# Kernel tuning notes

Measured on AMD Instinct MI355X. Metric: run time of the kernel, lower is better.

The kernel has to match this reference:

```python
import jax, jax.numpy as jnp
import numpy as np

S, B, D, H, E, K, FF = 1024, 8, 768, 12, 8, 2, 3072


def _ln(x, w, b, eps=1e-5):
    m = x.mean(-1, keepdims=True)
    v = ((x - m) ** 2).mean(-1, keepdims=True)
    return (x - m) / jnp.sqrt(v + eps) * w + b


def setup_inputs() -> dict:
    key = jax.random.key(0)
    ks = jax.random.split(key, 12)
    s = 0.02
    return {
        "x": jax.random.normal(ks[0], (S, B, D), dtype=jnp.float32),
        "ln1_w": jnp.ones((D,), jnp.float32),
        "ln1_b": jnp.zeros((D,), jnp.float32),
        "in_proj_w": jax.random.normal(ks[1], (3 * D, D), jnp.float32) * s,
        "in_proj_b": jnp.zeros((3 * D,), jnp.float32),
        "out_proj_w": jax.random.normal(ks[2], (D, D), jnp.float32) * s,
        "out_proj_b": jnp.zeros((D,), jnp.float32),
        "ln2_w": jnp.ones((D,), jnp.float32),
        "ln2_b": jnp.zeros((D,), jnp.float32),
        "gate_w": jax.random.normal(ks[3], (E, D), jnp.float32) * s,
        "w1": jax.random.normal(ks[4], (E, D, FF), jnp.float32) * s,
        "b1": jnp.zeros((E, FF), jnp.float32),
        "w2": jax.random.normal(ks[5], (E, FF, D), jnp.float32) * s,
        "b2": jnp.zeros((E, D), jnp.float32),
    }


def reference(x, ln1_w, ln1_b, in_proj_w, in_proj_b, out_proj_w, out_proj_b,
              ln2_w, ln2_b, gate_w, w1, b1, w2, b2):
    s, b, d = x.shape
    hd = d // H
    # --- self attention (nn.MultiheadAttention, seq-first, no mask) ---
    h = _ln(x, ln1_w, ln1_b)
    qkv = h @ in_proj_w.T + in_proj_b            # [S, B, 3D]
    q, k, v = jnp.split(qkv, 3, axis=-1)

    def heads(t):
        return t.reshape(s, b, H, hd).transpose(1, 2, 0, 3)  # [B, H, S, hd]

    q, k, v = heads(q) * (hd ** -0.5), heads(k), heads(v)
    att = jax.nn.softmax(jnp.einsum('bhqd,bhkd->bhqk', q, k), axis=-1)
    o = jnp.einsum('bhqk,bhkd->bhqd', att, v).transpose(2, 0, 1, 3).reshape(s, b, d)
    o = o @ out_proj_w.T + out_proj_b
    x = x + o
    # --- MoE FFN ---
    h2 = _ln(x, ln2_w, ln2_b)
    tok = h2.reshape(-1, d)                      # [T, D], T = S*B
    logits = tok @ gate_w.T                      # [T, E]
    rw = jax.nn.softmax(logits.astype(jnp.float32), axis=-1)
    rw_top, sel = jax.lax.top_k(rw, K)           # [T, K]
    rw_top = rw_top / rw_top.sum(-1, keepdims=True)
    rw_top = rw_top.astype(tok.dtype)
    out = jnp.zeros_like(tok)
    for e in range(E):  # small fixed expert loop; math matches gather/scatter dispatch
        we = jnp.where(sel == e, rw_top, 0.0).sum(-1)       # [T] combine weight
        mid = tok @ w1[e] + b1[e]
        mid = mid * jax.nn.sigmoid(1.702 * mid)              # QuickGELU
        out = out + we[:, None] * (mid @ w2[e] + b2[e])
    return x + out.reshape(s, b, d), logits
```

## Files before the change

kernel.cpp:

```cpp
#include <hip/hip_runtime.h>
#include <stdint.h>

#define S_LEN  1024
#define BATCH  8
#define DMODEL 768
#define NHEAD  12
#define HDIM   64
#define NEXP   8
#define FFDIM  3072
#define NTOK   8192
#define D3     2304
#define NGATH  16384
#define MAXWL  136

typedef unsigned short u16;
typedef unsigned int   u32;
typedef __attribute__((ext_vector_type(8))) short bf16x8;
typedef __attribute__((ext_vector_type(4))) float f32x4;
typedef __attribute__((ext_vector_type(4))) short s16x4;

__device__ __forceinline__ u16 f2bf(float f){
  u32 x = __float_as_uint(f);
  x += 0x7fffu + ((x >> 16) & 1u);
  return (u16)(x >> 16);
}
__device__ __forceinline__ float bf2f(u16 u){
  return __uint_as_float(((u32)u) << 16);
}
__device__ __forceinline__ u32 pkbf(float a, float b){
  u32 d; asm("v_cvt_pk_bf16_f32 %0, %1, %2" : "=v"(d) : "v"(a), "v"(b)); return d;
}
__device__ __forceinline__ void gl_lds16(const void* g, void* l){
  __builtin_amdgcn_global_load_lds(
      (const __attribute__((address_space(1))) u32*)(uintptr_t)g,
      (__attribute__((address_space(3))) u32*)(u32)(uintptr_t)l,
      16, 0, 0);
}
__device__ __forceinline__ int swz64(int r){ return ((r & 7) ^ ((r >> 3) & 7)) << 4; }

__device__ __forceinline__ int xcd_swz(int orig, int nwg){
  const int q = nwg >> 3, r = nwg & 7;
  const int xcd = orig & 7, loc = orig >> 3;
  return (xcd < r ? xcd * (q + 1) : r * (q + 1) + (xcd - r) * q) + loc;
}

__global__ __launch_bounds__(256)
void cvt_bf16(const float* __restrict__ in, u16* __restrict__ out, int n)
{
  int i = (blockIdx.x * 256 + threadIdx.x) * 4;
  if (i + 3 < n) {
    float4 v = *(const float4*)(in + i);
    out[i]     = f2bf(v.x);
    out[i + 1] = f2bf(v.y);
    out[i + 2] = f2bf(v.z);
    out[i + 3] = f2bf(v.w);
  }
}

__global__ __launch_bounds__(256)
void transpose_cvt(const float* __restrict__ in, u16* __restrict__ out, int rows, int cols)
{
  __shared__ float tile[64][65];
  const size_t eo = (size_t)blockIdx.z * rows * cols;
  in  += eo; out += eo;
  const int bx = blockIdx.x * 64;
  const int by = blockIdx.y * 64;
  const int tid = threadIdx.x;
  #pragma unroll
  for (int i = 0; i < 4; i++) {
    const int c = tid + 256 * i;
    const int r = c >> 4, c4 = (c & 15) * 4;
    const float4 v = *(const float4*)(in + (size_t)(by + r) * cols + bx + c4);
    tile[r][c4] = v.x; tile[r][c4 + 1] = v.y; tile[r][c4 + 2] = v.z; tile[r][c4 + 3] = v.w;
  }
  __syncthreads();
  #pragma unroll
  for (int i = 0; i < 4; i++) {
    const int c = tid + 256 * i;
    const int orow = c >> 4, r4 = (c & 15) * 4;
    uint2 p;
    p.x = pkbf(tile[r4][orow],     tile[r4 + 1][orow]);
    p.y = pkbf(tile[r4 + 2][orow], tile[r4 + 3][orow]);
    *(uint2*)(out + (size_t)(bx + orow) * rows + by + r4) = p;
  }
}

__global__ __launch_bounds__(256)
void ln_fwd(const float* __restrict__ x, const float* __restrict__ w, const float* __restrict__ b,
            u16* __restrict__ out)
{
  const int t = blockIdx.x, tid = threadIdx.x;
  const float* xr = x + (size_t)t * DMODEL;
  const float v0 = xr[tid], v1 = xr[tid + 256], v2 = xr[tid + 512];
  float s = v0 + v1 + v2, ss = v0 * v0 + v1 * v1 + v2 * v2;
  #pragma unroll
  for (int d = 1; d < 64; d <<= 1) { s += __shfl_xor(s, d); ss += __shfl_xor(ss, d); }
  __shared__ float rs[4], rq[4];
  if ((tid & 63) == 0) { rs[tid >> 6] = s; rq[tid >> 6] = ss; }
  __syncthreads();
  s  = rs[0] + rs[1] + rs[2] + rs[3];
  ss = rq[0] + rq[1] + rq[2] + rq[3];
  const float mean = s * (1.f / DMODEL);
  const float rstd = rsqrtf(ss * (1.f / DMODEL) - mean * mean + 1e-5f);
  u16* orow = out + (size_t)t * DMODEL;
  orow[tid]       = f2bf((v0 - mean) * rstd * w[tid]       + b[tid]);
  orow[tid + 256] = f2bf((v1 - mean) * rstd * w[tid + 256] + b[tid + 256]);
  orow[tid + 512] = f2bf((v2 - mean) * rstd * w[tid + 512] + b[tid + 512]);
}

__global__ __launch_bounds__(256)
void ln2_gate(const float* __restrict__ x1, const float* __restrict__ w, const float* __restrict__ b,
              const float* __restrict__ gate_w, u16* __restrict__ h2,
              float* __restrict__ logits, float* __restrict__ selw, int* __restrict__ seli)
{
  const int t = blockIdx.x, tid = threadIdx.x;
  const float* xr = x1 + (size_t)t * DMODEL;
  const float v0 = xr[tid], v1 = xr[tid + 256], v2 = xr[tid + 512];
  float s = v0 + v1 + v2, ss = v0 * v0 + v1 * v1 + v2 * v2;
  #pragma unroll
  for (int d = 1; d < 64; d <<= 1) { s += __shfl_xor(s, d); ss += __shfl_xor(ss, d); }
  __shared__ float rs[4], rq[4];
  if ((tid & 63) == 0) { rs[tid >> 6] = s; rq[tid >> 6] = ss; }
  __syncthreads();
  s  = rs[0] + rs[1] + rs[2] + rs[3];
  ss = rq[0] + rq[1] + rq[2] + rq[3];
  const float mean = s * (1.f / DMODEL);
  const float rstd = rsqrtf(ss * (1.f / DMODEL) - mean * mean + 1e-5f);
  __shared__ float row[DMODEL];
  const float y0 = (v0 - mean) * rstd * w[tid]       + b[tid];
  const float y1 = (v1 - mean) * rstd * w[tid + 256] + b[tid + 256];
  const float y2 = (v2 - mean) * rstd * w[tid + 512] + b[tid + 512];
  row[tid] = y0; row[tid + 256] = y1; row[tid + 512] = y2;
  u16* hr = h2 + (size_t)t * DMODEL;
  hr[tid] = f2bf(y0); hr[tid + 256] = f2bf(y1); hr[tid + 512] = f2bf(y2);
  __syncthreads();
  __shared__ float lg[NEXP];
  if (tid < 64) {
    const int e = tid >> 3, j = tid & 7;
    const float* gw = gate_w + e * DMODEL;
    float a = 0.f;
    for (int d = j; d < DMODEL; d += 8) a += row[d] * gw[d];
    a += __shfl_xor(a, 1); a += __shfl_xor(a, 2); a += __shfl_xor(a, 4);
    if (j == 0) lg[e] = a;
  }
  __syncthreads();
  if (tid < NEXP) logits[(size_t)t * NEXP + tid] = lg[tid];
  if (tid == 0) {
    int ia = 0, ib = -1;
    float va = -1e30f, vb = -1e30f;
    #pragma unroll
    for (int e = 0; e < NEXP; e++) {
      const float p = lg[e];
      if (p > va)      { vb = va; ib = ia; va = p; ia = e; }
      else if (p > vb) { vb = p; ib = e; }
    }
    const float pb = __expf(vb - va);
    const float inv = 1.f / (1.f + pb);
    selw[2 * t]     = inv;
    selw[2 * t + 1] = pb * inv;
    seli[2 * t]     = ia;
    seli[2 * t + 1] = ib;
  }
}

__global__ __launch_bounds__(256)
void route_count(const int* __restrict__ seli, int* __restrict__ blkcnt)
{
  __shared__ int c[NEXP];
  const int tid = threadIdx.x;
  if (tid < NEXP) c[tid] = 0;
  __syncthreads();
  const int t = blockIdx.x * 256 + tid;
  atomicAdd(&c[seli[2 * t]], 1);
  atomicAdd(&c[seli[2 * t + 1]], 1);
  __syncthreads();
  if (tid < NEXP) blkcnt[blockIdx.x * NEXP + tid] = c[tid];
}

__global__ void route_scan(const int* __restrict__ blkcnt, int* __restrict__ offs,
                           int* __restrict__ blkbase, int* __restrict__ wl, int* __restrict__ nwork)
{
  const int tid = threadIdx.x;
  __shared__ int tot[NEXP];
  __shared__ int off_s[NEXP + 1];
  if (tid < NEXP) {
    int s = 0;
    for (int blk = 0; blk < 32; blk++) s += blkcnt[blk * NEXP + tid];
    tot[tid] = s;
  }
  __syncthreads();
  if (tid == 0) {
    int run = 0;
    for (int e = 0; e < NEXP; e++) { off_s[e] = run; run += tot[e]; }
    off_s[NEXP] = run;
    int nw = 0;
    for (int e = 0; e < NEXP; e++) {
      const int nb = (tot[e] + 127) >> 7;
      for (int i2 = 0; i2 < nb; i2++) wl[nw++] = (e << 16) | i2;
    }
    nwork[0] = nw;
  }
  __syncthreads();
  if (tid <= NEXP) offs[tid] = off_s[tid];
  if (tid < NEXP) {
    int run = off_s[tid];
    for (int blk = 0; blk < 32; blk++) { blkbase[blk * NEXP + tid] = run; run += blkcnt[blk * NEXP + tid]; }
  }
}

__global__ __launch_bounds__(256)
void route_place(const int* __restrict__ seli, const int* __restrict__ blkbase,
                 int* __restrict__ perm, int* __restrict__ posmap)
{
  __shared__ int cnts[2][4][NEXP];
  __shared__ int base[NEXP];
  const int tid = threadIdx.x, l = tid & 63, w = tid >> 6, blk = blockIdx.x;
  const int t = blk * 256 + tid;
  const unsigned long long ltm = (1ull << l) - 1ull;
  int my_e[2], my_r[2];
  my_e[0] = seli[2 * t]; my_e[1] = seli[2 * t + 1];
  my_r[0] = 0; my_r[1] = 0;
  if (tid < NEXP) base[tid] = blkbase[blk * NEXP + tid];
  #pragma unroll
  for (int k = 0; k < 2; k++) {
    #pragma unroll
    for (int ee = 0; ee < NEXP; ee++) {
      const unsigned long long msk = __ballot(my_e[k] == ee);
      if (my_e[k] == ee) my_r[k] = (int)__popcll(msk & ltm);
      if (l == ee) cnts[k][w][ee] = (int)__popcll(msk);
    }
  }
  __syncthreads();
  #pragma unroll
  for (int k = 0; k < 2; k++) {
    const int e = my_e[k];
    int pre = base[e];
    for (int k2 = 0; k2 < 2; k2++)
      for (int w2 = 0; w2 < 4; w2++)
        if (k2 < k || (k2 == k && w2 < w)) pre += cnts[k2][w2][e];
    const int pos = pre + my_r[k];
    perm[pos] = t;
    posmap[2 * t + k] = pos;
  }
}

template<int MODE, int GRP>
__global__ __launch_bounds__(256)
void gemm128(const u16* __restrict__ A, const u16* __restrict__ Bw,
             int M, int N, int Kd,
             const float* __restrict__ bias, const float* __restrict__ resid,
             void* __restrict__ outp,
             const int* __restrict__ perm, const int* __restrict__ offs,
             const int* __restrict__ wl, const int* __restrict__ nwork)
{
  __shared__ u16 As[2][128 * 64];
  __shared__ u16 Bs[2][128 * 64];
  const int tid = threadIdx.x;
  const int l   = tid & 63;
  const int w   = tid >> 6;
  const int wm  = w >> 1, wn = w & 1;

  int gbase = 0, cnt = M, e = 0, bm, bn;
  if (MODE >= 2) {
    const int nw  = nwork[0];
    const int nwg = nw * (N >> 7);
    if ((int)blockIdx.x >= nwg) return;
    const int t    = xcd_swz(blockIdx.x, nwg);
    const int bnin = t % GRP;
    const int q    = t / GRP;
    const int bmi  = q % nw;
    bn = (q / nw) * GRP + bnin;
    const int wk = wl[bmi];
    e  = wk >> 16;
    bm = wk & 0xffff;
    gbase = offs[e];
    cnt   = offs[e + 1] - gbase;
  } else {
    const int nwm = M >> 7;
    const int t    = xcd_swz(blockIdx.x, gridDim.x);
    const int bnin = t % GRP;
    const int q    = t / GRP;
    bm = q % nwm;
    bn = (q / nwm) * GRP + bnin;
  }
  const u16*   Bp = Bw   + (MODE >= 2 ? (size_t)e * N * Kd : 0);
  const float* bp = bias + (MODE >= 2 ? e * N : 0);

  int arow[4], acol[4], brow[4];
  #pragma unroll
  for (int i = 0; i < 4; i++) {
    const int c = tid + 256 * i;
    const int r = c >> 3;
    const int f = (r & 7) ^ ((r >> 3) & 7);
    acol[i] = ((c & 7) ^ f) * 8;
    brow[i] = bn * 128 + r;
    int g;
    if (MODE == 2)      { int gp = gbase + bm * 128 + r; if (gp > NGATH - 1) gp = NGATH - 1; g = perm[gp]; }
    else if (MODE == 3) { int gp = gbase + bm * 128 + r; if (gp > NGATH - 1) gp = NGATH - 1; g = gp; }
    else                g = bm * 128 + r;
    arow[i] = g;
  }

  f32x4 acc[4][4] = {};
  const int nk = Kd >> 6;

  #pragma unroll
  for (int i = 0; i < 4; i++) {
    gl_lds16(A  + (size_t)arow[i] * Kd + acol[i], &As[0][(i * 256 + w * 64) * 8]);
    gl_lds16(Bp + (size_t)brow[i] * Kd + acol[i], &Bs[0][(i * 256 + w * 64) * 8]);
  }

  int cur = 0;
  for (int kt = 0; kt < nk; kt++) {
    const bool pf = (kt + 1 < nk);
    if (pf) {
      const int kb = (kt + 1) * 64;
      #pragma unroll
      for (int i = 0; i < 4; i++) {
        gl_lds16(A  + (size_t)arow[i] * Kd + kb + acol[i], &As[cur ^ 1][(i * 256 + w * 64) * 8]);
        gl_lds16(Bp + (size_t)brow[i] * Kd + kb + acol[i], &Bs[cur ^ 1][(i * 256 + w * 64) * 8]);
      }
      asm volatile("s_waitcnt vmcnt(8)" ::: "memory");
    } else {
      asm volatile("s_waitcnt vmcnt(0)" ::: "memory");
    }
    __builtin_amdgcn_s_barrier();
    __builtin_amdgcn_sched_barrier(0);

    #pragma unroll
    for (int ks = 0; ks < 2; ks++) {
      bf16x8 af[4], bv[4];
      #pragma unroll
      for (int m = 0; m < 4; m++) {
        const int row = wm * 64 + m * 16 + (l & 15);
        af[m] = *(const bf16x8*)((const char*)&As[cur][0] +
                  ((row * 128 + ks * 64 + (l >> 4) * 16) ^ swz64(row)));
      }
      #pragma unroll
      for (int n = 0; n < 4; n++) {
        const int row = wn * 64 + n * 16 + (l & 15);
        bv[n] = *(const bf16x8*)((const char*)&Bs[cur][0] +
                  ((row * 128 + ks * 64 + (l >> 4) * 16) ^ swz64(row)));
      }
      #pragma unroll
      for (int m = 0; m < 4; m++)
        #pragma unroll
        for (int n = 0; n < 4; n++)
          acc[m][n] = __builtin_amdgcn_mfma_f32_16x16x32_bf16(bv[n], af[m], acc[m][n], 0, 0, 0);
    }
    if (pf) __builtin_amdgcn_s_barrier();
    cur ^= 1;
  }

  f32x4 biasv[4];
  int   c0[4];
  #pragma unroll
  for (int n = 0; n < 4; n++) {
    c0[n] = bn * 128 + wn * 64 + n * 16 + ((l >> 4) << 2);
    biasv[n] = *(const f32x4*)(bp + c0[n]);
  }
  #pragma unroll
  for (int m = 0; m < 4; m++) {
    const int row = bm * 128 + wm * 64 + m * 16 + (l & 15);
    #pragma unroll
    for (int n = 0; n < 4; n++) {
      f32x4 v = acc[m][n] + biasv[n];
      if (MODE == 0) {
        *(uint2*)((u16*)outp + (size_t)row * N + c0[n]) =
            make_uint2(pkbf(v[0], v[1]), pkbf(v[2], v[3]));
      } else if (MODE == 1) {
        const size_t o = (size_t)row * N + c0[n];
        f32x4 rv = *(const f32x4*)(resid + o);
        v += rv;
        *(f32x4*)((float*)outp + o) = v;
      } else if (MODE == 2) {
        if (row < cnt) {
          #pragma unroll
          for (int r = 0; r < 4; r++)
            v[r] = v[r] * __builtin_amdgcn_rcpf(1.f + __expf(-1.702f * v[r]));
          *(uint2*)((u16*)outp + (size_t)(gbase + row) * FFDIM + c0[n]) =
              make_uint2(pkbf(v[0], v[1]), pkbf(v[2], v[3]));
        }
      } else {
        if (row < cnt)
          *(uint2*)((u16*)outp + (size_t)(gbase + row) * DMODEL + c0[n]) =
              make_uint2(pkbf(v[0], v[1]), pkbf(v[2], v[3]));
      }
    }
  }
}

__global__ __launch_bounds__(256)
void attn_fwd(const u16* __restrict__ qkv, u16* __restrict__ o)
{
  __shared__ u16 Ksw[64 * 64];
  __shared__ u16 Vt [64 * 64];
  __shared__ u16 Pl [4 * 16 * 64];
  const int tid = threadIdx.x;
  const int l   = tid & 63, w = tid >> 6;
  const int tt  = xcd_swz(blockIdx.x, 16 * BATCH * NHEAD);
  const int qt  = tt & 15;
  const int bh  = tt >> 4;
  const int b_  = bh / NHEAD;
  const int hh  = bh % NHEAD;

  const int qrow = qt * 64 + w * 16 + (l & 15);
  const size_t qoff = ((size_t)(qrow * BATCH + b_)) * D3 + hh * HDIM + (l >> 4) * 8;
  const bf16x8 qa0 = *(const bf16x8*)&qkv[qoff];
  const bf16x8 qa1 = *(const bf16x8*)&qkv[qoff + 32];

  f32x4 oacc[4] = {};
  float m_[4], l_[4];
  #pragma unroll
  for (int r = 0; r < 4; r++) { m_[r] = -1e30f; l_[r] = 0.f; }

  u16* Pw = Pl + w * 1024;
  const int pswz = swz64(l & 15);

  for (int kt = 0; kt < 16; kt++) {
    #pragma unroll
    for (int i = 0; i < 2; i++) {
      const int c = tid + 256 * i;
      const int key = c >> 3, dimb = (c & 7) * 8;
      const size_t gb = ((size_t)((kt * 64 + key) * BATCH + b_)) * D3 + hh * HDIM + dimb;
      const bf16x8 kd = *(const bf16x8*)&qkv[gb + DMODEL];
      const bf16x8 vd = *(const bf16x8*)&qkv[gb + 2 * DMODEL];
      *(bf16x8*)((char*)Ksw + ((key * 128 + dimb * 2) ^ swz64(key))) = kd;
      #pragma unroll
      for (int j = 0; j < 8; j++) {
        const int dim = dimb + j;
        *(u16*)((char*)Vt + ((dim * 128 + key * 2) ^ swz64(dim))) = (u16)vd[j];
      }
    }
    __syncthreads();

    f32x4 sc[4] = {};
    #pragma unroll
    for (int kb2 = 0; kb2 < 4; kb2++) {
      const int key = kb2 * 16 + (l & 15);
      const int ksz = swz64(key);
      #pragma unroll
      for (int ks = 0; ks < 2; ks++) {
        const bf16x8 kf = *(const bf16x8*)((char*)Ksw +
            ((key * 128 + (ks * 32 + (l >> 4) * 8) * 2) ^ ksz));
        sc[kb2] = __builtin_amdgcn_mfma_f32_16x16x32_bf16(ks ? qa1 : qa0, kf, sc[kb2], 0, 0, 0);
      }
    }
    #pragma unroll
    for (int kb2 = 0; kb2 < 4; kb2++)
      #pragma unroll
      for (int r = 0; r < 4; r++) sc[kb2][r] *= 0.125f;

    float nm[4], corr[4], ps[4];
    #pragma unroll
    for (int r = 0; r < 4; r++) {
      float pm = fmaxf(fmaxf(sc[0][r], sc[1][r]), fmaxf(sc[2][r], sc[3][r]));
      pm = fmaxf(pm, __shfl_xor(pm, 1));
      pm = fmaxf(pm, __shfl_xor(pm, 2));
      pm = fmaxf(pm, __shfl_xor(pm, 4));
      pm = fmaxf(pm, __shfl_xor(pm, 8));
      nm[r]   = fmaxf(m_[r], pm);
      corr[r] = __expf(m_[r] - nm[r]);
      m_[r]   = nm[r];
      ps[r]   = 0.f;
    }
    #pragma unroll
    for (int kb2 = 0; kb2 < 4; kb2++) {
      #pragma unroll
      for (int r = 0; r < 4; r++) {
        const float p = __expf(sc[kb2][r] - nm[r]);
        ps[r] += p;
        const int prow = (l >> 4) * 4 + r;
        const int pcol = kb2 * 16 + (l & 15);
        *(u16*)((char*)Pw + ((prow * 128 + pcol * 2) ^ swz64(prow))) = f2bf(p);
      }
    }
    #pragma unroll
    for (int r = 0; r < 4; r++) {
      float s = ps[r];
      s += __shfl_xor(s, 1); s += __shfl_xor(s, 2);
      s += __shfl_xor(s, 4); s += __shfl_xor(s, 8);
      l_[r] = l_[r] * corr[r] + s;
      #pragma unroll
      for (int ob = 0; ob < 4; ob++) oacc[ob][r] *= corr[r];
    }

    #pragma unroll
    for (int ob = 0; ob < 4; ob++) {
      const int dim = ob * 16 + (l & 15);
      const int vsz = swz64(dim);
      #pragma unroll
      for (int ks = 0; ks < 2; ks++) {
        const int kko = (ks * 32 + (l >> 4) * 8) * 2;
        const bf16x8 pf = *(const bf16x8*)((char*)Pw + (((l & 15) * 128 + kko) ^ pswz));
        const bf16x8 vf = *(const bf16x8*)((char*)Vt + ((dim * 128 + kko) ^ vsz));
        oacc[ob] = __builtin_amdgcn_mfma_f32_16x16x32_bf16(pf, vf, oacc[ob], 0, 0, 0);
      }
    }
    __syncthreads();
  }

  #pragma unroll
  for (int r = 0; r < 4; r++) {
    const float inv = 1.f / l_[r];
    const int qs = qt * 64 + w * 16 + (l >> 4) * 4 + r;
    #pragma unroll
    for (int ob = 0; ob < 4; ob++)
      o[((size_t)(qs * BATCH + b_)) * DMODEL + hh * HDIM + ob * 16 + (l & 15)] =
          f2bf(oacc[ob][r] * inv);
  }
}

__global__ __launch_bounds__(192)
void moe_combine(const float* __restrict__ x1, const u16* __restrict__ eout,
                 const int* __restrict__ posmap, const float* __restrict__ selw,
                 float* __restrict__ out)
{
  const int t = blockIdx.x, j = threadIdx.x;
  const int p0 = posmap[2 * t], p1 = posmap[2 * t + 1];
  const float w0 = selw[2 * t], w1 = selw[2 * t + 1];
  const float4 xv = ((const float4*)(x1 + (size_t)t * DMODEL))[j];
  const s16x4 a = ((const s16x4*)(eout + (size_t)p0 * DMODEL))[j];
  const s16x4 c = ((const s16x4*)(eout + (size_t)p1 * DMODEL))[j];
  float4 r;
  r.x = xv.x + w0 * bf2f((u16)a[0]) + w1 * bf2f((u16)c[0]);
  r.y = xv.y + w0 * bf2f((u16)a[1]) + w1 * bf2f((u16)c[1]);
  r.z = xv.z + w0 * bf2f((u16)a[2]) + w1 * bf2f((u16)c[2]);
  r.w = xv.w + w0 * bf2f((u16)a[3]) + w1 * bf2f((u16)c[3]);
  ((float4*)(out + (size_t)t * DMODEL))[j] = r;
}

#define MB (1ull << 20)
static const size_t OFF_H    = 0;
static const size_t OFF_QKV  = 16 * MB;
static const size_t OFF_O    = 54 * MB;
static const size_t OFF_IPW  = 67 * MB;
static const size_t OFF_OPW  = 71 * MB;
static const size_t OFF_MID  = 0;
static const size_t OFF_X1   = 101 * MB;
static const size_t OFF_H2   = 127 * MB;
static const size_t OFF_W1T  = 140 * MB;
static const size_t OFF_W2T  = 178 * MB;
static const size_t OFF_EOUT = 216 * MB;
static const size_t OFF_SELW = 242 * MB;
static const size_t OFF_PERM = 242 * MB + (1 << 16);
static const size_t OFF_POS  = 242 * MB + (2 << 16);
static const size_t OFF_SELI = 242 * MB + (3 << 16);
static const size_t OFF_BCNT = 242 * MB + (4 << 16);
static const size_t OFF_BBASE= 242 * MB + (4 << 16) + 4096;
static const size_t OFF_OFFS = 242 * MB + (4 << 16) + 8192;
static const size_t OFF_WL   = 242 * MB + (5 << 16);
static const size_t OFF_NW   = 242 * MB + (5 << 16) + 1024;

extern "C" void kernel_launch(void* const* d_in, const int* in_sizes, int n_in,
                              void* d_out, int out_size, void* d_ws, size_t ws_size,
                              hipStream_t stream)
{
  const float* x     = (const float*)d_in[0];
  const float* ln1w  = (const float*)d_in[1];
  const float* ln1b  = (const float*)d_in[2];
  const float* ipw_f = (const float*)d_in[3];
  const float* ipb   = (const float*)d_in[4];
  const float* opw_f = (const float*)d_in[5];
  const float* opb   = (const float*)d_in[6];
  const float* ln2w  = (const float*)d_in[7];
  const float* ln2b  = (const float*)d_in[8];
  const float* gatew = (const float*)d_in[9];
  const float* w1    = (const float*)d_in[10];
  const float* b1    = (const float*)d_in[11];
  const float* w2    = (const float*)d_in[12];
  const float* b2    = (const float*)d_in[13];

  char* ws = (char*)d_ws;
  u16*   h    = (u16*)(ws + OFF_H);
  u16*   qkv  = (u16*)(ws + OFF_QKV);
  u16*   ob   = (u16*)(ws + OFF_O);
  u16*   ipw  = (u16*)(ws + OFF_IPW);
  u16*   opw  = (u16*)(ws + OFF_OPW);
  u16*   mid  = (u16*)(ws + OFF_MID);
  float* x1   = (float*)(ws + OFF_X1);
  u16*   h2   = (u16*)(ws + OFF_H2);
  u16*   w1t  = (u16*)(ws + OFF_W1T);
  u16*   w2t  = (u16*)(ws + OFF_W2T);
  u16*   eout = (u16*)(ws + OFF_EOUT);
  float* selw = (float*)(ws + OFF_SELW);
  int*   perm = (int*)(ws + OFF_PERM);
  int*   posm = (int*)(ws + OFF_POS);
  int*   seli = (int*)(ws + OFF_SELI);
  int*   bcnt = (int*)(ws + OFF_BCNT);
  int*   bbas = (int*)(ws + OFF_BBASE);
  int*   offs = (int*)(ws + OFF_OFFS);
  int*   wl   = (int*)(ws + OFF_WL);
  int*   nwork= (int*)(ws + OFF_NW);
  float* outx  = (float*)d_out;
  float* outlg = outx + (size_t)NTOK * DMODEL;

  cvt_bf16<<<(D3 * DMODEL) / 1024, 256, 0, stream>>>(ipw_f, ipw, D3 * DMODEL);
  cvt_bf16<<<(DMODEL * DMODEL) / 1024, 256, 0, stream>>>(opw_f, opw, DMODEL * DMODEL);
  transpose_cvt<<<dim3(FFDIM / 64, DMODEL / 64, NEXP), 256, 0, stream>>>(w1, w1t, DMODEL, FFDIM);
  transpose_cvt<<<dim3(DMODEL / 64, FFDIM / 64, NEXP), 256, 0, stream>>>(w2, w2t, FFDIM, DMODEL);

  ln_fwd<<<NTOK, 256, 0, stream>>>(x, ln1w, ln1b, h);
  gemm128<0, 6><<<(NTOK / 128) * (D3 / 128), 256, 0, stream>>>(
      h, ipw, NTOK, D3, DMODEL, ipb, nullptr, qkv, nullptr, nullptr, nullptr, nullptr);
  attn_fwd<<<(S_LEN / 64) * BATCH * NHEAD, 256, 0, stream>>>(qkv, ob);
  gemm128<1, 6><<<(NTOK / 128) * (DMODEL / 128), 256, 0, stream>>>(
      ob, opw, NTOK, DMODEL, DMODEL, opb, x, x1, nullptr, nullptr, nullptr, nullptr);

  ln2_gate<<<NTOK, 256, 0, stream>>>(x1, ln2w, ln2b, gatew, h2, outlg, selw, seli);
  route_count<<<32, 256, 0, stream>>>(seli, bcnt);
  route_scan<<<1, 64, 0, stream>>>(bcnt, offs, bbas, wl, nwork);
  route_place<<<32, 256, 0, stream>>>(seli, bbas, perm, posm);

  gemm128<2, 12><<<MAXWL * (FFDIM / 128), 256, 0, stream>>>(
      h2, w1t, NGATH, FFDIM, DMODEL, b1, nullptr, mid, perm, offs, wl, nwork);
  gemm128<3, 6><<<MAXWL * (DMODEL / 128), 256, 0, stream>>>(
      mid, w2t, NGATH, DMODEL, FFDIM, b2, nullptr, eout, nullptr, offs, wl, nwork);

  moe_combine<<<NTOK, 192, 0, stream>>>(x1, eout, posm, selw, outx);
}
```

Before: 515.2 us.

## Use incremental GEMM load pointers, vectorize V transpose stores, retune MoE group size

The GEMM loader now precomputes per-thread A and B global pointers and advances them by 64 each k-step, replacing the per-iteration row*Kd address arithmetic. The attention kernel builds the transposed V tile by having each thread gather 8 keys for one dim with scalar global loads, then write one 16-byte LDS store instead of 8 scalar u16 stores. The second expert GEMM's block-swizzle group size changes from 6 to 3. Together these aim to cut address ALU work and LDS store count, at the cost of narrower, less coalesced global reads for V and different L2 reuse from the new grouping.

```diff
diff --git a/kernel.cpp b/kernel.cpp
--- a/kernel.cpp
+++ b/kernel.cpp
@@ -286,19 +286,20 @@
   const u16*   Bp = Bw   + (MODE >= 2 ? (size_t)e * N * Kd : 0);
   const float* bp = bias + (MODE >= 2 ? e * N : 0);
 
-  int arow[4], acol[4], brow[4];
+  const u16* pa[4];
+  const u16* pb[4];
   #pragma unroll
   for (int i = 0; i < 4; i++) {
     const int c = tid + 256 * i;
     const int r = c >> 3;
     const int f = (r & 7) ^ ((r >> 3) & 7);
-    acol[i] = ((c & 7) ^ f) * 8;
-    brow[i] = bn * 128 + r;
+    const int col = ((c & 7) ^ f) * 8;
     int g;
     if (MODE == 2)      { int gp = gbase + bm * 128 + r; if (gp > NGATH - 1) gp = NGATH - 1; g = perm[gp]; }
     else if (MODE == 3) { int gp = gbase + bm * 128 + r; if (gp > NGATH - 1) gp = NGATH - 1; g = gp; }
     else                g = bm * 128 + r;
-    arow[i] = g;
+    pa[i] = A  + (size_t)g * Kd + col;
+    pb[i] = Bp + (size_t)(bn * 128 + r) * Kd + col;
   }
 
   f32x4 acc[4][4] = {};
@@ -306,19 +307,19 @@
 
   #pragma unroll
   for (int i = 0; i < 4; i++) {
-    gl_lds16(A  + (size_t)arow[i] * Kd + acol[i], &As[0][(i * 256 + w * 64) * 8]);
-    gl_lds16(Bp + (size_t)brow[i] * Kd + acol[i], &Bs[0][(i * 256 + w * 64) * 8]);
+    gl_lds16(pa[i], &As[0][(i * 256 + w * 64) * 8]);
+    gl_lds16(pb[i], &Bs[0][(i * 256 + w * 64) * 8]);
   }
 
   int cur = 0;
   for (int kt = 0; kt < nk; kt++) {
     const bool pf = (kt + 1 < nk);
     if (pf) {
-      const int kb = (kt + 1) * 64;
       #pragma unroll
       for (int i = 0; i < 4; i++) {
-        gl_lds16(A  + (size_t)arow[i] * Kd + kb + acol[i], &As[cur ^ 1][(i * 256 + w * 64) * 8]);
-        gl_lds16(Bp + (size_t)brow[i] * Kd + kb + acol[i], &Bs[cur ^ 1][(i * 256 + w * 64) * 8]);
+        pa[i] += 64; pb[i] += 64;
+        gl_lds16(pa[i], &As[cur ^ 1][(i * 256 + w * 64) * 8]);
+        gl_lds16(pb[i], &Bs[cur ^ 1][(i * 256 + w * 64) * 8]);
       }
       asm volatile("s_waitcnt vmcnt(8)" ::: "memory");
     } else {
@@ -424,13 +425,18 @@
       const int key = c >> 3, dimb = (c & 7) * 8;
       const size_t gb = ((size_t)((kt * 64 + key) * BATCH + b_)) * D3 + hh * HDIM + dimb;
       const bf16x8 kd = *(const bf16x8*)&qkv[gb + DMODEL];
-      const bf16x8 vd = *(const bf16x8*)&qkv[gb + 2 * DMODEL];
       *(bf16x8*)((char*)Ksw + ((key * 128 + dimb * 2) ^ swz64(key))) = kd;
-      #pragma unroll
-      for (int j = 0; j < 8; j++) {
-        const int dim = dimb + j;
-        *(u16*)((char*)Vt + ((dim * 128 + key * 2) ^ swz64(dim))) = (u16)vd[j];
-      }
+    }
+    #pragma unroll
+    for (int i = 0; i < 2; i++) {
+      const int dim = tid & 63;
+      const int kg  = (tid >> 6) + 4 * i;
+      const size_t vb = ((size_t)((kt * 64 + kg * 8) * BATCH + b_)) * D3 + 2 * DMODEL + hh * HDIM + dim;
+      bf16x8 vv;
+      #pragma unroll
+      for (int j = 0; j < 8; j++)
+        vv[j] = (short)qkv[vb + (size_t)j * BATCH * D3];
+      *(bf16x8*)((char*)Vt + ((dim * 128 + kg * 16) ^ swz64(dim))) = vv;
     }
     __syncthreads();
 
@@ -614,7 +620,7 @@
 
   gemm128<2, 12><<<MAXWL * (FFDIM / 128), 256, 0, stream>>>(
       h2, w1t, NGATH, FFDIM, DMODEL, b1, nullptr, mid, perm, offs, wl, nwork);
-  gemm128<3, 6><<<MAXWL * (DMODEL / 128), 256, 0, stream>>>(
+  gemm128<3, 3><<<MAXWL * (DMODEL / 128), 256, 0, stream>>>(
       mid, w2t, NGATH, DMODEL, FFDIM, b2, nullptr, eout, nullptr, offs, wl, nwork);
 
   moe_combine<<<NTOK, 192, 0, stream>>>(x1, eout, posm, selw, outx);
```

Result: no change. 516.1 us (+0.2%).
